# Kernel tuning notes

Hardware: AMD Instinct MI355X
Metric: run time of the kernel (lower is better)

The kernel has to match this reference:

```python
import jax, jax.numpy as jnp
import numpy as np

K = 4                      # options['num_k']
NOISE_EPS = 0.1            # noise_epsilon in noisy_top_k_gating
LOSS_COEF = 1e-4
EPS_COMBINE = float(np.finfo(np.float64).eps)  # np.finfo(float).eps in combine
INV_SQRT2 = 0.7071067811865475


def _norm_cdf(z):
    # Normal(0,1).cdf
    return 0.5 * (1.0 + jax.lax.erf(z * INV_SQRT2))


def _cv_squared(v):
    # torch .var() is unbiased (ddof=1)
    return jnp.var(v, ddof=1) / (jnp.mean(v) ** 2 + 1e-10)


def setup_inputs() -> dict:
    key = jax.random.key(0)
    B, D, E, H, O = 1024, 1024, 16, 2048, 1024
    ks = jax.random.split(key, 6)
    x = jax.random.normal(ks[0], (B, D), jnp.float32)
    w_gate = jax.random.normal(ks[1], (D, E), jnp.float32) * 0.02
    w_noise = jax.random.normal(ks[2], (D, E), jnp.float32) * 0.02
    W1 = jax.random.normal(ks[3], (E, D, H), jnp.float32) / np.sqrt(D).astype(np.float32)
    b1 = jnp.zeros((E, H), jnp.float32)
    W2 = jax.random.normal(ks[4], (E, H, O), jnp.float32) / np.sqrt(H).astype(np.float32)
    b2 = jnp.zeros((E, O), jnp.float32)
    noise = jax.random.normal(ks[5], (B, E), jnp.float32)  # randn_like(clean_logits)
    return {"x": x, "w_gate": w_gate, "w_noise": w_noise,
            "W1": W1, "b1": b1, "W2": W2, "b2": b2, "noise": noise}


def moe_forward(x, w_gate, w_noise, W1, b1, W2, b2, noise):
    B = x.shape[0]
    # --- noisy top-k gating (train=True path) ---
    clean_logits = x @ w_gate                              # [B, E]
    noise_std = jax.nn.softplus(x @ w_noise) + NOISE_EPS   # [B, E]
    noisy_logits = clean_logits + noise * noise_std        # [B, E]
    top_logits, top_idx = jax.lax.top_k(noisy_logits, K + 1)  # [B, K+1]
    topk_gates = jax.nn.softmax(top_logits[:, :K], axis=1)    # [B, K]
    gates = jnp.zeros_like(noisy_logits).at[
        jnp.arange(B)[:, None], top_idx[:, :K]].set(topk_gates)  # [B, E] sparse
    # --- load = E[prob in top-k] (smooth load estimate) ---
    thr_in = top_logits[:, K][:, None]       # (k+1)-th value: threshold if in
    thr_out = top_logits[:, K - 1][:, None]  # k-th value: threshold if out
    is_in = noisy_logits > thr_in
    prob_if_in = _norm_cdf((clean_logits - thr_in) / noise_std)
    prob_if_out = _norm_cdf((clean_logits - thr_out) / noise_std)
    load = jnp.where(is_in, prob_if_in, prob_if_out).sum(0)   # [E]
    importance = gates.sum(0)                                 # [E]
    loss = (_cv_squared(importance) + _cv_squared(load)) * LOSS_COEF
    # --- experts + combine ---
    # Dense all-expert compute; gates are exactly zero off the top-k so the
    # gate-weighted sum reproduces the sparse dispatch/index_add combine math.
    h = jax.nn.relu(jnp.einsum('bi,eih->beh', x, W1) + b1)    # [B, E, H]
    expert_out = jnp.einsum('beh,eho->beo', h, W2) + b2       # [B, E, O]
    # combine: sum_e gate[b,e] * exp(expert_out[b,e,:]); zeros -> eps; log
    combined = jnp.einsum('be,beo->bo', gates, jnp.exp(expert_out))  # [B, O]
    combined = jnp.where(combined == 0, EPS_COMBINE, combined)
    y = jnp.log(combined)
    return y, loss


def reference(x, w_gate, w_noise, W1, b1, W2, b2, noise):
    return moe_forward(x, w_gate, w_noise, W1, b1, W2, b2, noise)
```

## Files before the change

kernel.cpp:

```cpp
#include <hip/hip_runtime.h>
#include <cstdint>
#include <cstddef>

#define BTOK 1024
#define DDIM 1024
#define EEXP 16
#define HDIM 2048
#define ODIM 1024

typedef __bf16 bh;
typedef bh bh8 __attribute__((ext_vector_type(8)));
typedef bh bh4 __attribute__((ext_vector_type(4)));
typedef float fx4 __attribute__((ext_vector_type(4)));

__device__ __forceinline__ void gload16(const void* g, void* l) {
  __builtin_amdgcn_global_load_lds(
      (const __attribute__((address_space(1))) void*)g,
      (__attribute__((address_space(3))) void*)l, 16, 0, 0);
}

__global__ __launch_bounds__(256) void k_tcvt(const float* __restrict__ in,
                                              bh* __restrict__ out, int R, int C) {
  const int e = blockIdx.z;
  const int r0 = blockIdx.y * 64, c0 = blockIdx.x * 64;
  const float* pin = in + (size_t)e * R * C;
  bh* pout = out + (size_t)e * R * C;
  __shared__ __align__(16) bh t[64 * 65];
  const int tid = threadIdx.x;
#pragma unroll
  for (int rep = 0; rep < 4; ++rep) {
    int task = rep * 256 + tid;
    int r = task >> 4, c4 = task & 15;
    fx4 v = *(const fx4*)(pin + (size_t)(r0 + r) * C + c0 + c4 * 4);
    int base = r * 65 + c4 * 4;
#pragma unroll
    for (int u = 0; u < 4; ++u) t[base + u] = (bh)v[u];
  }
  __syncthreads();
#pragma unroll
  for (int rep = 0; rep < 4; ++rep) {
    int task = rep * 256 + tid;
    int cc = task >> 4, g2 = task & 15;
    bh4 o;
#pragma unroll
    for (int u = 0; u < 4; ++u) o[u] = t[(g2 * 4 + u) * 65 + cc];
    *(bh4*)(pout + (size_t)(c0 + cc) * R + r0 + g2 * 4) = o;
  }
}

__global__ __launch_bounds__(256) void k_gating(
    const float* __restrict__ x, const float* __restrict__ wg,
    const float* __restrict__ wn, const float* __restrict__ nz,
    bh* __restrict__ xbf, unsigned* __restrict__ cnt,
    int* __restrict__ tok_buck, float* __restrict__ gate_buck,
    float* __restrict__ imp_part, float* __restrict__ load_part) {
  const int b = blockIdx.x, tid = threadIdx.x;
  __shared__ __align__(16) float xs[1024];
  __shared__ float part[32][9];
  __shared__ float vals[32];
  fx4 v = *(const fx4*)(x + (size_t)b * 1024 + tid * 4);
  *(fx4*)(xs + tid * 4) = v;
  bh4 xb;
#pragma unroll
  for (int u = 0; u < 4; ++u) xb[u] = (bh)v[u];
  *(bh4*)(xbf + (size_t)b * 1024 + tid * 4) = xb;
  __syncthreads();
  const int col = tid & 31, g = tid >> 5;
  const float* wp = ((col < 16) ? wg : wn) + (col & 15);
  float s = 0.f;
  for (int it = g * 128; it < g * 128 + 128; ++it) s += xs[it] * wp[it * 16];
  part[col][g] = s;
  __syncthreads();
  if (tid < 32) {
    float tsum = 0.f;
#pragma unroll
    for (int gg = 0; gg < 8; ++gg) tsum += part[tid][gg];
    vals[tid] = tsum;
  }
  __syncthreads();
  if (tid == 0) {
    float clean[16], sd[16], noisy[16];
#pragma unroll
    for (int e = 0; e < 16; ++e) {
      clean[e] = vals[e];
      float raw = vals[16 + e];
      float sp = fmaxf(raw, 0.f) + log1pf(expf(-fabsf(raw)));
      sd[e] = sp + 0.1f;
      noisy[e] = clean[e] + nz[b * 16 + e] * sd[e];
    }
    float tv[5]; int ti[5]; unsigned used = 0;
    for (int r = 0; r < 5; ++r) {
      float bst = -INFINITY; int bi = 0;
      for (int e = 0; e < 16; ++e)
        if (!((used >> e) & 1u) && noisy[e] > bst) { bst = noisy[e]; bi = e; }
      used |= 1u << bi; tv[r] = bst; ti[r] = bi;
    }
    float gts[4]; float se = 0.f;
#pragma unroll
    for (int k = 0; k < 4; ++k) { gts[k] = expf(tv[k] - tv[0]); se += gts[k]; }
#pragma unroll
    for (int k = 0; k < 4; ++k) gts[k] /= se;
    const float thr_in = tv[4], thr_out = tv[3];
    float imp[16];
#pragma unroll
    for (int e = 0; e < 16; ++e) imp[e] = 0.f;
    for (int k = 0; k < 4; ++k) imp[ti[k]] = gts[k];
    for (int e = 0; e < 16; ++e) imp_part[b * 16 + e] = imp[e];
    for (int e = 0; e < 16; ++e) {
      bool is_in = noisy[e] > thr_in;
      float z = (clean[e] - (is_in ? thr_in : thr_out)) / sd[e];
      load_part[b * 16 + e] = 0.5f * (1.f + erff(z * 0.70710678118654752f));
    }
    for (int k = 0; k < 4; ++k) {
      int ee = ti[k];
      unsigned p = atomicAdd(&cnt[ee], 1u);
      tok_buck[ee * 1024 + (int)p] = b;
      gate_buck[ee * 1024 + (int)p] = gts[k];
    }
  }
}

__device__ __forceinline__ float cv2_16(const float* v) {
  float m = 0.f;
  for (int i = 0; i < 16; ++i) m += v[i];
  m *= (1.f / 16.f);
  float var = 0.f;
  for (int i = 0; i < 16; ++i) { float d = v[i] - m; var += d * d; }
  var *= (1.f / 15.f);
  return var / (m * m + 1e-10f);
}

__global__ __launch_bounds__(256) void k_finalize(
    const unsigned* __restrict__ cnt, unsigned* __restrict__ offs,
    const float* __restrict__ imp_part, const float* __restrict__ load_part,
    float* __restrict__ loss_out) {
  const int tid = threadIdx.x;
  __shared__ float red[256];
  __shared__ float impv[16], loadv[16];
  const int e = tid & 15, p = tid >> 4;
  float s = 0.f;
  for (int r = 0; r < 64; ++r) s += imp_part[((p * 64 + r) << 4) + e];
  red[tid] = s;
  __syncthreads();
  if (tid < 16) {
    float t = 0.f;
    for (int pp = 0; pp < 16; ++pp) t += red[pp * 16 + tid];
    impv[tid] = t;
  }
  __syncthreads();
  s = 0.f;
  for (int r = 0; r < 64; ++r) s += load_part[((p * 64 + r) << 4) + e];
  red[tid] = s;
  __syncthreads();
  if (tid < 16) {
    float t = 0.f;
    for (int pp = 0; pp < 16; ++pp) t += red[pp * 16 + tid];
    loadv[tid] = t;
  }
  __syncthreads();
  if (tid == 0) {
    unsigned o = 0;
    for (int ee = 0; ee < 16; ++ee) { offs[ee] = o; o += cnt[ee]; }
    loss_out[0] = (cv2_16(impv) + cv2_16(loadv)) * 1e-4f;
  }
}

__global__ __launch_bounds__(256) void k_gemm1(
    const bh* __restrict__ xbf, const bh* __restrict__ w1t,
    const float* __restrict__ b1, const int* __restrict__ tok_buck,
    const unsigned* __restrict__ cnt, const unsigned* __restrict__ offs,
    bh* __restrict__ hbf) {
  const int e = blockIdx.z, mt = blockIdx.y, nt = blockIdx.x;
  const int ne = (int)cnt[e];
  if (mt * 128 >= ne) return;
  __shared__ __align__(16) bh As[128 * 32];
  __shared__ __align__(16) bh Bs[128 * 32];
  const int tid = threadIdx.x;
  const int lane = tid & 63, wv = tid >> 6, wm = wv >> 1, wn_ = wv & 1;

  const bh* a_src[2]; const bh* b_src[2];
  void* a_dst[2]; void* b_dst[2];
#pragma unroll
  for (int r = 0; r < 2; ++r) {
    int task = r * 256 + tid;
    int row = task >> 2, s = task & 3;
    int gm = mt * 128 + row; if (gm >= ne) gm = ne - 1;
    int tok = tok_buck[e * 1024 + gm];
    a_src[r] = xbf + (size_t)tok * 1024 + ((s ^ (row & 3)) << 3);
    b_src[r] = w1t + (size_t)e * (2048 * 1024) + (size_t)(nt * 128 + row) * 1024 +
               ((s ^ (row & 3)) << 3);
    int wub = (r * 256 + (wv << 6)) << 4;
    a_dst[r] = (char*)As + wub;
    b_dst[r] = (char*)Bs + wub;
  }
  const int ln15 = lane & 15, q = lane >> 4;
  const int qs = ((q ^ (ln15 & 3)) << 3);
  int a_off[4], b_off[4];
#pragma unroll
  for (int i = 0; i < 4; ++i) {
    a_off[i] = (wm * 64 + i * 16 + ln15) * 32 + qs;
    b_off[i] = (wn_ * 64 + i * 16 + ln15) * 32 + qs;
  }
  fx4 zero = {0.f, 0.f, 0.f, 0.f};
  fx4 acc[4][4];
#pragma unroll
  for (int i = 0; i < 4; ++i)
#pragma unroll
    for (int j = 0; j < 4; ++j) acc[i][j] = zero;

  for (int kt = 0; kt < 32; ++kt) {
    __syncthreads();
    const int ko = kt * 32;
#pragma unroll
    for (int r = 0; r < 2; ++r) {
      gload16(a_src[r] + ko, a_dst[r]);
      gload16(b_src[r] + ko, b_dst[r]);
    }
    __syncthreads();
    bh8 af[4], bfr[4];
#pragma unroll
    for (int i = 0; i < 4; ++i) af[i] = *(const bh8*)(As + a_off[i]);
#pragma unroll
    for (int i = 0; i < 4; ++i) bfr[i] = *(const bh8*)(Bs + b_off[i]);
#pragma unroll
    for (int i = 0; i < 4; ++i)
#pragma unroll
      for (int j = 0; j < 4; ++j)
        acc[i][j] = __builtin_amdgcn_mfma_f32_16x16x32_bf16(af[i], bfr[j], acc[i][j], 0, 0, 0);
  }

  int nrows = ne - mt * 128; if (nrows > 128) nrows = 128;
  int jn[4]; float b1v[4];
#pragma unroll
  for (int j = 0; j < 4; ++j) {
    jn[j] = nt * 128 + wn_ * 64 + j * 16 + ln15;
    b1v[j] = b1[e * 2048 + jn[j]];
  }
  const int rowbase = (int)offs[e] + mt * 128;
#pragma unroll
  for (int i = 0; i < 4; ++i)
#pragma unroll
    for (int rr = 0; rr < 4; ++rr) {
      int ml = wm * 64 + i * 16 + q * 4 + rr;
      if (ml < nrows) {
        size_t ro = (size_t)(rowbase + ml) * 2048;
#pragma unroll
        for (int j = 0; j < 4; ++j) {
          float vv = acc[i][j][rr] + b1v[j];
          hbf[ro + jn[j]] = (bh)fmaxf(vv, 0.f);
        }
      }
    }
}

__global__ __launch_bounds__(256) void k_gemm2(
    const bh* __restrict__ hbf, const bh* __restrict__ w2t,
    const float* __restrict__ b2, const int* __restrict__ tok_buck,
    const float* __restrict__ gate_buck, const unsigned* __restrict__ cnt,
    const unsigned* __restrict__ offs, float* __restrict__ yv) {
  const int e = blockIdx.z, mt = blockIdx.y, nt = blockIdx.x;
  const int ne = (int)cnt[e];
  if (mt * 128 >= ne) return;
  __shared__ __align__(16) bh As[128 * 32];
  __shared__ __align__(16) bh Bs[128 * 32];
  const int tid = threadIdx.x;
  const int lane = tid & 63, wv = tid >> 6, wm = wv >> 1, wn_ = wv & 1;
  const int rowbase = (int)offs[e] + mt * 128;

  const bh* a_src[2]; const bh* b_src[2];
  void* a_dst[2]; void* b_dst[2];
#pragma unroll
  for (int r = 0; r < 2; ++r) {
    int task = r * 256 + tid;
    int row = task >> 2, s = task & 3;
    a_src[r] = hbf + (size_t)(rowbase + row) * 2048 + ((s ^ (row & 3)) << 3);
    b_src[r] = w2t + (size_t)e * (1024 * 2048) + (size_t)(nt * 128 + row) * 2048 +
               ((s ^ (row & 3)) << 3);
    int wub = (r * 256 + (wv << 6)) << 4;
    a_dst[r] = (char*)As + wub;
    b_dst[r] = (char*)Bs + wub;
  }
  const int ln15 = lane & 15, q = lane >> 4;
  const int qs = ((q ^ (ln15 & 3)) << 3);
  int a_off[4], b_off[4];
#pragma unroll
  for (int i = 0; i < 4; ++i) {
    a_off[i] = (wm * 64 + i * 16 + ln15) * 32 + qs;
    b_off[i] = (wn_ * 64 + i * 16 + ln15) * 32 + qs;
  }
  fx4 zero = {0.f, 0.f, 0.f, 0.f};
  fx4 acc[4][4];
#pragma unroll
  for (int i = 0; i < 4; ++i)
#pragma unroll
    for (int j = 0; j < 4; ++j) acc[i][j] = zero;

  for (int kt = 0; kt < 64; ++kt) {
    __syncthreads();
    const int ko = kt * 32;
#pragma unroll
    for (int r = 0; r < 2; ++r) {
      gload16(a_src[r] + ko, a_dst[r]);
      gload16(b_src[r] + ko, b_dst[r]);
    }
    __syncthreads();
    bh8 af[4], bfr[4];
#pragma unroll
    for (int i = 0; i < 4; ++i) af[i] = *(const bh8*)(As + a_off[i]);
#pragma unroll
    for (int i = 0; i < 4; ++i) bfr[i] = *(const bh8*)(Bs + b_off[i]);
#pragma unroll
    for (int i = 0; i < 4; ++i)
#pragma unroll
      for (int j = 0; j < 4; ++j)
        acc[i][j] = __builtin_amdgcn_mfma_f32_16x16x32_bf16(af[i], bfr[j], acc[i][j], 0, 0, 0);
  }

  int nrows = ne - mt * 128; if (nrows > 128) nrows = 128;
  int on[4]; float b2v[4];
#pragma unroll
  for (int j = 0; j < 4; ++j) {
    on[j] = nt * 128 + wn_ * 64 + j * 16 + ln15;
    b2v[j] = b2[e * 1024 + on[j]];
  }
#pragma unroll
  for (int i = 0; i < 4; ++i)
#pragma unroll
    for (int rr = 0; rr < 4; ++rr) {
      int ml = wm * 64 + i * 16 + q * 4 + rr;
      if (ml < nrows) {
        int pos = mt * 128 + ml;
        int bt = tok_buck[e * 1024 + pos];
        float gg = gate_buck[e * 1024 + pos];
        float* yrow = yv + (size_t)bt * 1024;
#pragma unroll
        for (int j = 0; j < 4; ++j)
          atomicAdd(&yrow[on[j]], gg * expf(acc[i][j][rr] + b2v[j]));
      }
    }
}

__global__ __launch_bounds__(256) void k_log(float* __restrict__ yv) {
  const int i = blockIdx.x * 256 + threadIdx.x;
  fx4* p = (fx4*)yv + i;
  fx4 v = *p;
#pragma unroll
  for (int c = 0; c < 4; ++c) {
    float w = v[c];
    if (w == 0.f) w = 2.2204460492503131e-16f;
    v[c] = logf(w);
  }
  *p = v;
}

extern "C" void kernel_launch(void* const* d_in, const int* in_sizes, int n_in,
                              void* d_out, int out_size, void* d_ws, size_t ws_size,
                              hipStream_t stream) {
  const float* x  = (const float*)d_in[0];
  const float* wg = (const float*)d_in[1];
  const float* wn = (const float*)d_in[2];
  const float* W1 = (const float*)d_in[3];
  const float* b1 = (const float*)d_in[4];
  const float* W2 = (const float*)d_in[5];
  const float* b2 = (const float*)d_in[6];
  const float* nz = (const float*)d_in[7];
  float* out = (float*)d_out;

  char* ws = (char*)d_ws;
  unsigned* cnt      = (unsigned*)(ws + 0);
  unsigned* offs     = (unsigned*)(ws + 64);
  float*    imp_part = (float*)(ws + 256);
  float*    load_part= (float*)(ws + 256 + 65536);
  int*      tok_buck = (int*)(ws + 256 + 2 * 65536);
  float*    gate_buck= (float*)(ws + 256 + 3 * 65536);
  bh*       xbf      = (bh*)(ws + 262400);
  bh*       hbf      = (bh*)(ws + 2359552);
  bh*       w1t      = (bh*)(ws + 19661056);
  bh*       w2t      = (bh*)(ws + 86769920);
  const size_t needed = 153878784;
  if (ws_size < needed) {
    hipMemsetAsync(d_out, 0x42, (size_t)out_size * 4, stream);
    return;
  }

  hipMemsetAsync(d_out, 0, (size_t)out_size * 4, stream);
  hipMemsetAsync(cnt, 0, 64, stream);

  k_tcvt<<<dim3(2048 / 64, 1024 / 64, 16), 256, 0, stream>>>(W1, w1t, 1024, 2048);
  k_tcvt<<<dim3(1024 / 64, 2048 / 64, 16), 256, 0, stream>>>(W2, w2t, 2048, 1024);
  k_gating<<<1024, 256, 0, stream>>>(x, wg, wn, nz, xbf, cnt, tok_buck, gate_buck,
                                     imp_part, load_part);
  k_finalize<<<1, 256, 0, stream>>>(cnt, offs, imp_part, load_part, out + (out_size - 1));
  k_gemm1<<<dim3(16, 8, 16), 256, 0, stream>>>(xbf, w1t, b1, tok_buck, cnt, offs, hbf);
  k_gemm2<<<dim3(8, 8, 16), 256, 0, stream>>>(hbf, w2t, b2, tok_buck, gate_buck, cnt, offs, out);
  k_log<<<1024, 256, 0, stream>>>(out);
}
```

Baseline: 489.1 us.

## Add 4-stage LDS ring with prefetch-ahead global loads in expert GEMMs

Both expert GEMM kernels replace the single-buffered load, sync, compute loop with a 4-deep LDS ring buffer. Global-to-LDS loads run three k-tiles ahead, and explicit vmcnt waits plus one barrier per iteration replace the two __syncthreads. This is meant to hide global memory latency behind MFMA work. In exchange, LDS use per block grows from 16KB to 64KB, which may lower occupancy, and correctness depends on the hand-written waitcnt counts.

```diff
diff --git a/kernel.cpp b/kernel.cpp
--- a/kernel.cpp
+++ b/kernel.cpp
@@ -173,13 +173,13 @@
   const int e = blockIdx.z, mt = blockIdx.y, nt = blockIdx.x;
   const int ne = (int)cnt[e];
   if (mt * 128 >= ne) return;
-  __shared__ __align__(16) bh As[128 * 32];
-  __shared__ __align__(16) bh Bs[128 * 32];
+  __shared__ __align__(16) bh As[4][128 * 32];
+  __shared__ __align__(16) bh Bs[4][128 * 32];
   const int tid = threadIdx.x;
   const int lane = tid & 63, wv = tid >> 6, wm = wv >> 1, wn_ = wv & 1;
 
   const bh* a_src[2]; const bh* b_src[2];
-  void* a_dst[2]; void* b_dst[2];
+  int dst_off[2];
 #pragma unroll
   for (int r = 0; r < 2; ++r) {
     int task = r * 256 + tid;
@@ -189,9 +189,7 @@
     a_src[r] = xbf + (size_t)tok * 1024 + ((s ^ (row & 3)) << 3);
     b_src[r] = w1t + (size_t)e * (2048 * 1024) + (size_t)(nt * 128 + row) * 1024 +
                ((s ^ (row & 3)) << 3);
-    int wub = (r * 256 + (wv << 6)) << 4;
-    a_dst[r] = (char*)As + wub;
-    b_dst[r] = (char*)Bs + wub;
+    dst_off[r] = (r * 256 + (wv << 6)) << 4;
   }
   const int ln15 = lane & 15, q = lane >> 4;
   const int qs = ((q ^ (ln15 & 3)) << 3);
@@ -208,25 +206,38 @@
 #pragma unroll
     for (int j = 0; j < 4; ++j) acc[i][j] = zero;
 
-  for (int kt = 0; kt < 32; ++kt) {
-    __syncthreads();
+  auto stage = [&](int qb, int kt) {
     const int ko = kt * 32;
 #pragma unroll
     for (int r = 0; r < 2; ++r) {
-      gload16(a_src[r] + ko, a_dst[r]);
-      gload16(b_src[r] + ko, b_dst[r]);
-    }
-    __syncthreads();
+      gload16(a_src[r] + ko, (char*)(&As[qb][0]) + dst_off[r]);
+      gload16(b_src[r] + ko, (char*)(&Bs[qb][0]) + dst_off[r]);
+    }
+  };
+
+  const int NT = 32;
+  stage(0, 0); stage(1, 1); stage(2, 2);
+  asm volatile("s_waitcnt vmcnt(8)" ::: "memory");
+  __builtin_amdgcn_s_barrier();
+
+  for (int t = 0; t < NT; ++t) {
+    if (t + 3 < NT) stage((t + 3) & 3, t + 3);
+    const bh* Ab = &As[t & 3][0];
+    const bh* Bb = &Bs[t & 3][0];
     bh8 af[4], bfr[4];
 #pragma unroll
-    for (int i = 0; i < 4; ++i) af[i] = *(const bh8*)(As + a_off[i]);
-#pragma unroll
-    for (int i = 0; i < 4; ++i) bfr[i] = *(const bh8*)(Bs + b_off[i]);
+    for (int i = 0; i < 4; ++i) af[i] = *(const bh8*)(Ab + a_off[i]);
+#pragma unroll
+    for (int i = 0; i < 4; ++i) bfr[i] = *(const bh8*)(Bb + b_off[i]);
 #pragma unroll
     for (int i = 0; i < 4; ++i)
 #pragma unroll
       for (int j = 0; j < 4; ++j)
         acc[i][j] = __builtin_amdgcn_mfma_f32_16x16x32_bf16(af[i], bfr[j], acc[i][j], 0, 0, 0);
+    if (t + 3 < NT)      asm volatile("s_waitcnt vmcnt(8) lgkmcnt(0)" ::: "memory");
+    else if (t + 2 < NT) asm volatile("s_waitcnt vmcnt(4) lgkmcnt(0)" ::: "memory");
+    else if (t + 1 < NT) asm volatile("s_waitcnt vmcnt(0) lgkmcnt(0)" ::: "memory");
+    if (t + 1 < NT) __builtin_amdgcn_s_barrier();
   }
 
   int nrows = ne - mt * 128; if (nrows > 128) nrows = 128;
@@ -261,14 +272,14 @@
   const int e = blockIdx.z, mt = blockIdx.y, nt = blockIdx.x;
   const int ne = (int)cnt[e];
   if (mt * 128 >= ne) return;
-  __shared__ __align__(16) bh As[128 * 32];
-  __shared__ __align__(16) bh Bs[128 * 32];
+  __shared__ __align__(16) bh As[4][128 * 32];
+  __shared__ __align__(16) bh Bs[4][128 * 32];
   const int tid = threadIdx.x;
   const int lane = tid & 63, wv = tid >> 6, wm = wv >> 1, wn_ = wv & 1;
   const int rowbase = (int)offs[e] + mt * 128;
 
   const bh* a_src[2]; const bh* b_src[2];
-  void* a_dst[2]; void* b_dst[2];
+  int dst_off[2];
 #pragma unroll
   for (int r = 0; r < 2; ++r) {
     int task = r * 256 + tid;
@@ -276,9 +287,7 @@
     a_src[r] = hbf + (size_t)(rowbase + row) * 2048 + ((s ^ (row & 3)) << 3);
     b_src[r] = w2t + (size_t)e * (1024 * 2048) + (size_t)(nt * 128 + row) * 2048 +
                ((s ^ (row & 3)) << 3);
-    int wub = (r * 256 + (wv << 6)) << 4;
-    a_dst[r] = (char*)As + wub;
-    b_dst[r] = (char*)Bs + wub;
+    dst_off[r] = (r * 256 + (wv << 6)) << 4;
   }
   const int ln15 = lane & 15, q = lane >> 4;
   const int qs = ((q ^ (ln15 & 3)) << 3);
@@ -295,25 +304,38 @@
 #pragma unroll
     for (int j = 0; j < 4; ++j) acc[i][j] = zero;
 
-  for (int kt = 0; kt < 64; ++kt) {
-    __syncthreads();
+  auto stage = [&](int qb, int kt) {
     const int ko = kt * 32;
 #pragma unroll
     for (int r = 0; r < 2; ++r) {
-      gload16(a_src[r] + ko, a_dst[r]);
-      gload16(b_src[r] + ko, b_dst[r]);
-    }
-    __syncthreads();
+      gload16(a_src[r] + ko, (char*)(&As[qb][0]) + dst_off[r]);
+      gload16(b_src[r] + ko, (char*)(&Bs[qb][0]) + dst_off[r]);
+    }
+  };
+
+  const int NT = 64;
+  stage(0, 0); stage(1, 1); stage(2, 2);
+  asm volatile("s_waitcnt vmcnt(8)" ::: "memory");
+  __builtin_amdgcn_s_barrier();
+
+  for (int t = 0; t < NT; ++t) {
+    if (t + 3 < NT) stage((t + 3) & 3, t + 3);
+    const bh* Ab = &As[t & 3][0];
+    const bh* Bb = &Bs[t & 3][0];
     bh8 af[4], bfr[4];
 #pragma unroll
-    for (int i = 0; i < 4; ++i) af[i] = *(const bh8*)(As + a_off[i]);
-#pragma unroll
-    for (int i = 0; i < 4; ++i) bfr[i] = *(const bh8*)(Bs + b_off[i]);
+    for (int i = 0; i < 4; ++i) af[i] = *(const bh8*)(Ab + a_off[i]);
+#pragma unroll
+    for (int i = 0; i < 4; ++i) bfr[i] = *(const bh8*)(Bb + b_off[i]);
 #pragma unroll
     for (int i = 0; i < 4; ++i)
 #pragma unroll
       for (int j = 0; j < 4; ++j)
         acc[i][j] = __builtin_amdgcn_mfma_f32_16x16x32_bf16(af[i], bfr[j], acc[i][j], 0, 0, 0);
+    if (t + 3 < NT)      asm volatile("s_waitcnt vmcnt(8) lgkmcnt(0)" ::: "memory");
+    else if (t + 2 < NT) asm volatile("s_waitcnt vmcnt(4) lgkmcnt(0)" ::: "memory");
+    else if (t + 1 < NT) asm volatile("s_waitcnt vmcnt(0) lgkmcnt(0)" ::: "memory");
+    if (t + 1 < NT) __builtin_amdgcn_s_barrier();
   }
 
   int nrows = ne - mt * 128; if (nrows > 128) nrows = 128;
```

New measurement: 502.7 us. +2.8%, slower.

## Fuse fp32-to-bf16 weight conversion into expert GEMMs with 4-stage pipeline

Applied to the files above, without the earlier changes.

Drops the separate transpose/convert kernels that turned W1 and W2 into bf16 copies in workspace. The GEMMs now load fp32 weights straight into registers, convert them to bf16 and write them to LDS, inside a 4-buffer software pipeline that uses explicit waitcnt and barriers to overlap loads with MFMA work. This removes a full extra read and write pass over the weights and two launches. In exchange, each GEMM tile reads fp32 weights (twice the bytes) more than once across token tiles, and the kernels use more LDS and registers, which can lower occupancy.

```diff
diff --git a/kernel.cpp b/kernel.cpp
--- a/kernel.cpp
+++ b/kernel.cpp
@@ -17,35 +17,6 @@
   __builtin_amdgcn_global_load_lds(
       (const __attribute__((address_space(1))) void*)g,
       (__attribute__((address_space(3))) void*)l, 16, 0, 0);
-}
-
-__global__ __launch_bounds__(256) void k_tcvt(const float* __restrict__ in,
-                                              bh* __restrict__ out, int R, int C) {
-  const int e = blockIdx.z;
-  const int r0 = blockIdx.y * 64, c0 = blockIdx.x * 64;
-  const float* pin = in + (size_t)e * R * C;
-  bh* pout = out + (size_t)e * R * C;
-  __shared__ __align__(16) bh t[64 * 65];
-  const int tid = threadIdx.x;
-#pragma unroll
-  for (int rep = 0; rep < 4; ++rep) {
-    int task = rep * 256 + tid;
-    int r = task >> 4, c4 = task & 15;
-    fx4 v = *(const fx4*)(pin + (size_t)(r0 + r) * C + c0 + c4 * 4);
-    int base = r * 65 + c4 * 4;
-#pragma unroll
-    for (int u = 0; u < 4; ++u) t[base + u] = (bh)v[u];
-  }
-  __syncthreads();
-#pragma unroll
-  for (int rep = 0; rep < 4; ++rep) {
-    int task = rep * 256 + tid;
-    int cc = task >> 4, g2 = task & 15;
-    bh4 o;
-#pragma unroll
-    for (int u = 0; u < 4; ++u) o[u] = t[(g2 * 4 + u) * 65 + cc];
-    *(bh4*)(pout + (size_t)(c0 + cc) * R + r0 + g2 * 4) = o;
-  }
 }
 
 __global__ __launch_bounds__(256) void k_gating(
@@ -165,21 +136,108 @@
   }
 }
 
+
+#define SBAR0() __builtin_amdgcn_sched_barrier(0)
+#define WAITV(N) asm volatile("s_waitcnt vmcnt(" #N ")" ::: "memory")
+#define WAITL() asm volatile("s_waitcnt lgkmcnt(0)" ::: "memory")
+
+#define B_LOAD(SLOT, T) do {                                        \
+  const float* bp_ = bsrc + (size_t)(T) * (32 * BRS);               \
+  _Pragma("unroll") for (int kk_ = 0; kk_ < 16; ++kk_)              \
+    br[SLOT][kk_] = bp_[(size_t)kk_ * BRS];                         \
+} while (0)
+
+#define A_STAGE(BUF, T) do {                                        \
+  int ko_ = (T) * 32;                                               \
+  gload16(a_src[0] + ko_, (char*)(&As[BUF][0]) + dst_off[0]);       \
+  gload16(a_src[1] + ko_, (char*)(&As[BUF][0]) + dst_off[1]);       \
+} while (0)
+
+#define B_CVTW(SLOT, BUF) do {                                      \
+  bh8 w0_, w1_;                                                     \
+  _Pragma("unroll") for (int u_ = 0; u_ < 8; ++u_) {                \
+    w0_[u_] = (bh)br[SLOT][u_]; w1_[u_] = (bh)br[SLOT][8 + u_]; }   \
+  *(bh8*)(&Bs[BUF][(size_t)bq0 * 1024 + bn8]) = w0_;                \
+  *(bh8*)(&Bs[BUF][(size_t)(bq0 + 1) * 1024 + bn8]) = w1_;          \
+} while (0)
+
+#define COMPUTE(BUF) do {                                           \
+  bh8 af_[4], bf_[4];                                               \
+  _Pragma("unroll") for (int i_ = 0; i_ < 4; ++i_)                  \
+    af_[i_] = *(const bh8*)(&As[BUF][a_off[i_]]);                   \
+  _Pragma("unroll") for (int i_ = 0; i_ < 4; ++i_)                  \
+    bf_[i_] = *(const bh8*)(&Bs[BUF][(size_t)(q * 128 + wn_ * 64 + i_ * 16 + ln15) * 8]); \
+  _Pragma("unroll") for (int i_ = 0; i_ < 4; ++i_)                  \
+    _Pragma("unroll") for (int j_ = 0; j_ < 4; ++j_)                \
+      acc[i_][j_] = __builtin_amdgcn_mfma_f32_16x16x32_bf16(af_[i_], bf_[j_], acc[i_][j_], 0, 0, 0); \
+} while (0)
+
+#define KSTEP_STD(T, K) do {                                        \
+  B_LOAD(((K) + 2) & 3, (T) + 2);                                   \
+  A_STAGE(((K) + 3) & 3, (T) + 3);                                  \
+  SBAR0();                                                          \
+  COMPUTE((K));                                                     \
+  WAITV(18);                                                        \
+  B_CVTW(((K) + 1) & 3, ((K) + 1) & 3);                             \
+  WAITL();                                                          \
+  __builtin_amdgcn_s_barrier();                                     \
+} while (0)
+
+#define KSTEP_T3(T, K) do {               \
+  B_LOAD(((K) + 2) & 3, (T) + 2);                                   \
+  SBAR0();                                                          \
+  COMPUTE((K));                                                     \
+  WAITV(16);                                                        \
+  B_CVTW(((K) + 1) & 3, ((K) + 1) & 3);                             \
+  WAITL();                                                          \
+  __builtin_amdgcn_s_barrier();                                     \
+} while (0)
+
+#define KSTEP_T2(K) do {                   \
+  COMPUTE((K));                                                     \
+  WAITV(0);                                                         \
+  B_CVTW(((K) + 1) & 3, ((K) + 1) & 3);                             \
+  WAITL();                                                          \
+  __builtin_amdgcn_s_barrier();                                     \
+} while (0)
+
+#define KSTEP_LAST(K) do { COMPUTE((K)); } while (0)
+
+#define GEMM_PROLOGUE() do {                                        \
+  B_LOAD(0, 0); A_STAGE(0, 0); SBAR0();                             \
+  B_LOAD(1, 1); A_STAGE(1, 1); A_STAGE(2, 2); SBAR0();              \
+  WAITV(20);                                                        \
+  B_CVTW(0, 0);                                                     \
+  WAITL();                                                          \
+  __builtin_amdgcn_s_barrier();                                     \
+} while (0)
+
+#define GEMM_MAIN(NT) do {                                          \
+  for (int tb = 0; tb + 8 <= (NT); tb += 4) {                       \
+    KSTEP_STD(tb + 0, 0); KSTEP_STD(tb + 1, 1);                     \
+    KSTEP_STD(tb + 2, 2); KSTEP_STD(tb + 3, 3);                     \
+  }                                                                 \
+  KSTEP_STD((NT) - 4, 0);                                           \
+  KSTEP_T3((NT) - 3, 1);                                            \
+  KSTEP_T2(2);                                                      \
+  KSTEP_LAST(3);                                                    \
+} while (0)
+
 __global__ __launch_bounds__(256) void k_gemm1(
-    const bh* __restrict__ xbf, const bh* __restrict__ w1t,
+    const bh* __restrict__ xbf, const float* __restrict__ W1,
     const float* __restrict__ b1, const int* __restrict__ tok_buck,
     const unsigned* __restrict__ cnt, const unsigned* __restrict__ offs,
     bh* __restrict__ hbf) {
   const int e = blockIdx.z, mt = blockIdx.y, nt = blockIdx.x;
   const int ne = (int)cnt[e];
   if (mt * 128 >= ne) return;
-  __shared__ __align__(16) bh As[128 * 32];
-  __shared__ __align__(16) bh Bs[128 * 32];
+  __shared__ __align__(16) bh As[4][128 * 32];
+  __shared__ __align__(16) bh Bs[4][128 * 32];
   const int tid = threadIdx.x;
   const int lane = tid & 63, wv = tid >> 6, wm = wv >> 1, wn_ = wv & 1;
-
-  const bh* a_src[2]; const bh* b_src[2];
-  void* a_dst[2]; void* b_dst[2];
+  const int BRS = HDIM;
+
+  const bh* a_src[2]; int dst_off[2];
 #pragma unroll
   for (int r = 0; r < 2; ++r) {
     int task = r * 256 + tid;
@@ -187,20 +245,21 @@
     int gm = mt * 128 + row; if (gm >= ne) gm = ne - 1;
     int tok = tok_buck[e * 1024 + gm];
     a_src[r] = xbf + (size_t)tok * 1024 + ((s ^ (row & 3)) << 3);
-    b_src[r] = w1t + (size_t)e * (2048 * 1024) + (size_t)(nt * 128 + row) * 1024 +
-               ((s ^ (row & 3)) << 3);
-    int wub = (r * 256 + (wv << 6)) << 4;
-    a_dst[r] = (char*)As + wub;
-    b_dst[r] = (char*)Bs + wub;
-  }
+    dst_off[r] = (r * 256 + (wv << 6)) << 4;
+  }
+  const int bcol = nt * 128 + (tid & 127);
+  const int khalf = (tid >> 7) * 16;
+  const int bq0 = (tid >> 7) * 2;
+  const int bn8 = (tid & 127) * 8;
+  const float* bsrc = W1 + (size_t)e * (DDIM * HDIM) + (size_t)khalf * BRS + bcol;
+  float br[4][16];
+
   const int ln15 = lane & 15, q = lane >> 4;
   const int qs = ((q ^ (ln15 & 3)) << 3);
-  int a_off[4], b_off[4];
-#pragma unroll
-  for (int i = 0; i < 4; ++i) {
-    a_off[i] = (wm * 64 + i * 16 + ln15) * 32 + qs;
-    b_off[i] = (wn_ * 64 + i * 16 + ln15) * 32 + qs;
-  }
+  int a_off[4];
+#pragma unroll
+  for (int i = 0; i < 4; ++i) a_off[i] = (wm * 64 + i * 16 + ln15) * 32 + qs;
+
   fx4 zero = {0.f, 0.f, 0.f, 0.f};
   fx4 acc[4][4];
 #pragma unroll
@@ -208,26 +267,8 @@
 #pragma unroll
     for (int j = 0; j < 4; ++j) acc[i][j] = zero;
 
-  for (int kt = 0; kt < 32; ++kt) {
-    __syncthreads();
-    const int ko = kt * 32;
-#pragma unroll
-    for (int r = 0; r < 2; ++r) {
-      gload16(a_src[r] + ko, a_dst[r]);
-      gload16(b_src[r] + ko, b_dst[r]);
-    }
-    __syncthreads();
-    bh8 af[4], bfr[4];
-#pragma unroll
-    for (int i = 0; i < 4; ++i) af[i] = *(const bh8*)(As + a_off[i]);
-#pragma unroll
-    for (int i = 0; i < 4; ++i) bfr[i] = *(const bh8*)(Bs + b_off[i]);
-#pragma unroll
-    for (int i = 0; i < 4; ++i)
-#pragma unroll
-      for (int j = 0; j < 4; ++j)
-        acc[i][j] = __builtin_amdgcn_mfma_f32_16x16x32_bf16(af[i], bfr[j], acc[i][j], 0, 0, 0);
-  }
+  GEMM_PROLOGUE();
+  GEMM_MAIN(32);
 
   int nrows = ne - mt * 128; if (nrows > 128) nrows = 128;
   int jn[4]; float b1v[4];
@@ -254,40 +295,41 @@
 }
 
 __global__ __launch_bounds__(256) void k_gemm2(
-    const bh* __restrict__ hbf, const bh* __restrict__ w2t,
+    const bh* __restrict__ hbf, const float* __restrict__ W2,
     const float* __restrict__ b2, const int* __restrict__ tok_buck,
     const float* __restrict__ gate_buck, const unsigned* __restrict__ cnt,
     const unsigned* __restrict__ offs, float* __restrict__ yv) {
   const int e = blockIdx.z, mt = blockIdx.y, nt = blockIdx.x;
   const int ne = (int)cnt[e];
   if (mt * 128 >= ne) return;
-  __shared__ __align__(16) bh As[128 * 32];
-  __shared__ __align__(16) bh Bs[128 * 32];
+  __shared__ __align__(16) bh As[4][128 * 32];
+  __shared__ __align__(16) bh Bs[4][128 * 32];
   const int tid = threadIdx.x;
   const int lane = tid & 63, wv = tid >> 6, wm = wv >> 1, wn_ = wv & 1;
   const int rowbase = (int)offs[e] + mt * 128;
-
-  const bh* a_src[2]; const bh* b_src[2];
-  void* a_dst[2]; void* b_dst[2];
+  const int BRS = ODIM;
+
+  const bh* a_src[2]; int dst_off[2];
 #pragma unroll
   for (int r = 0; r < 2; ++r) {
     int task = r * 256 + tid;
     int row = task >> 2, s = task & 3;
     a_src[r] = hbf + (size_t)(rowbase + row) * 2048 + ((s ^ (row & 3)) << 3);
-    b_src[r] = w2t + (size_t)e * (1024 * 2048) + (size_t)(nt * 128 + row) * 2048 +
-               ((s ^ (row & 3)) << 3);
-    int wub = (r * 256 + (wv << 6)) << 4;
-    a_dst[r] = (char*)As + wub;
-    b_dst[r] = (char*)Bs + wub;
-  }
+    dst_off[r] = (r * 256 + (wv << 6)) << 4;
+  }
+  const int bcol = nt * 128 + (tid & 127);
+  const int khalf = (tid >> 7) * 16;
+  const int bq0 = (tid >> 7) * 2;
+  const int bn8 = (tid & 127) * 8;
+  const float* bsrc = W2 + (size_t)e * (HDIM * ODIM) + (size_t)khalf * BRS + bcol;
+  float br[4][16];
+
   const int ln15 = lane & 15, q = lane >> 4;
   const int qs = ((q ^ (ln15 & 3)) << 3);
-  int a_off[4], b_off[4];
-#pragma unroll
-  for (int i = 0; i < 4; ++i) {
-    a_off[i] = (wm * 64 + i * 16 + ln15) * 32 + qs;
-    b_off[i] = (wn_ * 64 + i * 16 + ln15) * 32 + qs;
-  }
+  int a_off[4];
+#pragma unroll
+  for (int i = 0; i < 4; ++i) a_off[i] = (wm * 64 + i * 16 + ln15) * 32 + qs;
+
   fx4 zero = {0.f, 0.f, 0.f, 0.f};
   fx4 acc[4][4];
 #pragma unroll
@@ -295,26 +337,8 @@
 #pragma unroll
     for (int j = 0; j < 4; ++j) acc[i][j] = zero;
 
-  for (int kt = 0; kt < 64; ++kt) {
-    __syncthreads();
-    const int ko = kt * 32;
-#pragma unroll
-    for (int r = 0; r < 2; ++r) {
-      gload16(a_src[r] + ko, a_dst[r]);
-      gload16(b_src[r] + ko, b_dst[r]);
-    }
-    __syncthreads();
-    bh8 af[4], bfr[4];
-#pragma unroll
-    for (int i = 0; i < 4; ++i) af[i] = *(const bh8*)(As + a_off[i]);
-#pragma unroll
-    for (int i = 0; i < 4; ++i) bfr[i] = *(const bh8*)(Bs + b_off[i]);
-#pragma unroll
-    for (int i = 0; i < 4; ++i)
-#pragma unroll
-      for (int j = 0; j < 4; ++j)
-        acc[i][j] = __builtin_amdgcn_mfma_f32_16x16x32_bf16(af[i], bfr[j], acc[i][j], 0, 0, 0);
-  }
+  GEMM_PROLOGUE();
+  GEMM_MAIN(64);
 
   int nrows = ne - mt * 128; if (nrows > 128) nrows = 128;
   int on[4]; float b2v[4];
@@ -375,9 +399,7 @@
   float*    gate_buck= (float*)(ws + 256 + 3 * 65536);
   bh*       xbf      = (bh*)(ws + 262400);
   bh*       hbf      = (bh*)(ws + 2359552);
-  bh*       w1t      = (bh*)(ws + 19661056);
-  bh*       w2t      = (bh*)(ws + 86769920);
-  const size_t needed = 153878784;
+  const size_t needed = 19661056;
   if (ws_size < needed) {
     hipMemsetAsync(d_out, 0x42, (size_t)out_size * 4, stream);
     return;
@@ -386,12 +408,10 @@
   hipMemsetAsync(d_out, 0, (size_t)out_size * 4, stream);
   hipMemsetAsync(cnt, 0, 64, stream);
 
-  k_tcvt<<<dim3(2048 / 64, 1024 / 64, 16), 256, 0, stream>>>(W1, w1t, 1024, 2048);
-  k_tcvt<<<dim3(1024 / 64, 2048 / 64, 16), 256, 0, stream>>>(W2, w2t, 2048, 1024);
   k_gating<<<1024, 256, 0, stream>>>(x, wg, wn, nz, xbf, cnt, tok_buck, gate_buck,
                                      imp_part, load_part);
   k_finalize<<<1, 256, 0, stream>>>(cnt, offs, imp_part, load_part, out + (out_size - 1));
-  k_gemm1<<<dim3(16, 8, 16), 256, 0, stream>>>(xbf, w1t, b1, tok_buck, cnt, offs, hbf);
-  k_gemm2<<<dim3(8, 8, 16), 256, 0, stream>>>(hbf, w2t, b2, tok_buck, gate_buck, cnt, offs, out);
+  k_gemm1<<<dim3(16, 8, 16), 256, 0, stream>>>(xbf, W1, b1, tok_buck, cnt, offs, hbf);
+  k_gemm2<<<dim3(8, 8, 16), 256, 0, stream>>>(hbf, W2, b2, tok_buck, gate_buck, cnt, offs, out);
   k_log<<<1024, 256, 0, stream>>>(out);
 }
```

New measurement: 470.6 us. 3.8% less time.
